# Kernel optimization log

Hardware: AMD Instinct MI355X
Metric: run time of the kernel (lower is better)

## Reference

```python
import jax, jax.numpy as jnp
import numpy as np
from jax import lax

DIM = 192
HEADS = 8
EPS = 1e-5


def setup_inputs() -> dict:
    key = jax.random.key(0)
    ks = jax.random.split(key, 8)
    B, C, H, W = 1, DIM, 64, 64
    x = jax.random.normal(ks[0], (B, C, H, W), dtype=jnp.float32)
    gamma = jnp.ones((C,), dtype=jnp.float32)
    beta = jnp.zeros((C,), dtype=jnp.float32)
    w_qkv = jax.random.normal(ks[1], (3 * C, C), dtype=jnp.float32) * (1.0 / np.sqrt(C))
    # depthwise 3x3 conv: (out_ch=3C, in_ch/groups=1, 3, 3), bias present (Conv2d default)
    w_dw = jax.random.normal(ks[2], (3 * C, 1, 3, 3), dtype=jnp.float32) * (1.0 / 3.0)
    b_dw = jax.random.normal(ks[3], (3 * C,), dtype=jnp.float32) * 0.01
    w_proj = jax.random.normal(ks[4], (C, C), dtype=jnp.float32) * (1.0 / np.sqrt(C))
    temperature = jnp.ones((HEADS, 1, 1), dtype=jnp.float32)
    return {"x": x, "gamma": gamma, "beta": beta, "w_qkv": w_qkv,
            "w_dw": w_dw, "b_dw": b_dw, "w_proj": w_proj,
            "temperature": temperature}


def _mdta(x, gamma, beta, w_qkv, w_dw, b_dw, w_proj, temperature):
    B, C, H, W = x.shape
    heads = HEADS
    d = C // heads
    N = H * W
    # LayerNorm over channel dim (applied on NHWC permute in torch)
    mean = jnp.mean(x, axis=1, keepdims=True)
    var = jnp.var(x, axis=1, keepdims=True)
    x_ln = (x - mean) * lax.rsqrt(var + EPS)
    x_ln = x_ln * gamma[None, :, None, None] + beta[None, :, None, None]
    # 1x1 conv (no bias): [B,3C,H,W]
    qkv = jnp.einsum('oc,bchw->bohw', w_qkv, x_ln)
    # depthwise 3x3 conv, padding=1, groups=3C
    qkv = lax.conv_general_dilated(
        qkv, w_dw, window_strides=(1, 1), padding=((1, 1), (1, 1)),
        dimension_numbers=('NCHW', 'OIHW', 'NCHW'),
        feature_group_count=3 * C)
    qkv = qkv + b_dw[None, :, None, None]
    q, k, v = jnp.split(qkv, 3, axis=1)
    q = q.reshape(B, heads, d, N)
    k = k.reshape(B, heads, d, N)
    v = v.reshape(B, heads, d, N)
    # attn[b,h,n,m] = sum_d q[b,h,d,n] k[b,h,d,m], scaled by learnable temperature
    attn = jnp.einsum('bhdn,bhdm->bhnm', q, k) * temperature  # (heads,1,1) broadcasts
    attn = jax.nn.softmax(attn, axis=-1)
    # out[b,h,d,n] = sum_m attn[b,h,n,m] v[b,h,d,m]
    out = jnp.einsum('bhnm,bhdm->bhdn', attn, v)
    out = out.reshape(B, C, H, W)
    out = jnp.einsum('oc,bchw->bohw', w_proj, out)
    return out + x


def reference(x, gamma, beta, w_qkv, w_dw, b_dw, w_proj, temperature):
    return _mdta(x, gamma, beta, w_qkv, w_dw, b_dw, w_proj, temperature)
```

## Files before the change

kernel.cpp:

```cpp
#include <hip/hip_runtime.h>
#include <hip/hip_bf16.h>


typedef __bf16 bf16;
typedef __bf16 bf16x2 __attribute__((ext_vector_type(2)));
typedef __bf16 bf16x4 __attribute__((ext_vector_type(4)));
typedef __bf16 bf16x8 __attribute__((ext_vector_type(8)));
typedef float f32x4 __attribute__((ext_vector_type(4)));

#define C_DIM 192
#define N_PIX 4096
#define HEADS 8
#define DHEAD 24
#define DPAD 32
#define C3 576
#define NSPLIT 8

__device__ inline float fast_exp2(float x) {
#if __has_builtin(__builtin_amdgcn_exp2f)
    return __builtin_amdgcn_exp2f(x);
#else
    return exp2f(x);
#endif
}

__device__ inline f32x4 mfma16(bf16x8 a, bf16x8 b, f32x4 c) {
    return __builtin_amdgcn_mfma_f32_16x16x32_bf16(a, b, c, 0, 0, 0);
}

__global__ __launch_bounds__(256) void ln_qkv(const float* __restrict__ x,
                                              const float* __restrict__ gamma,
                                              const float* __restrict__ beta,
                                              const float* __restrict__ wqkv,
                                              bf16* __restrict__ qkvb,
                                              float* __restrict__ maxk2) {
    __shared__ __align__(16) bf16 Bt[64 * 200];
    __shared__ float gs[C_DIM], bs[C_DIM];
    const int K = C_DIM;
    int n0 = blockIdx.x * 64;
    int m0 = blockIdx.y * 64;
    int t = threadIdx.x;
    if (t < C_DIM) { gs[t] = gamma[t]; bs[t] = beta[t]; }
    if (blockIdx.x == 0 && blockIdx.y == 0 && t < 8) maxk2[t] = 0.0f;
    __syncthreads();

    int lane = t & 63, wave = t >> 6;
    {
        int pl = wave * 16 + (lane & 15);
        int seg = lane >> 4;
        int p = n0 + pl;
        float v[48];
        float s = 0.f, ss = 0.f;
        for (int j = 0; j < 48; ++j) {
            float f = x[(seg * 48 + j) * N_PIX + p];
            v[j] = f; s += f; ss += f * f;
        }
        s += __shfl_xor(s, 16, 64); s += __shfl_xor(s, 32, 64);
        ss += __shfl_xor(ss, 16, 64); ss += __shfl_xor(ss, 32, 64);
        float mean = s * (1.0f / C_DIM);
        float var = ss * (1.0f / C_DIM) - mean * mean;
        float rstd = rsqrtf(var + 1e-5f);
        bf16* dst = Bt + pl * 200 + seg * 48;
        for (int g = 0; g < 6; ++g) {
            bf16x8 w;
            for (int j = 0; j < 8; ++j) {
                int c = seg * 48 + g * 8 + j;
                w[j] = (bf16)((v[g * 8 + j] - mean) * rstd * gs[c] + bs[c]);
            }
            *(bf16x8*)(dst + g * 8) = w;
        }
    }
    __syncthreads();

    int l16 = lane & 15, quad = lane >> 4;
    int wm = (wave >> 1) * 32, wn = (wave & 1) * 32;
    f32x4 acc[2][2] = {};
    for (int kk = 0; kk < K; kk += 32) {
        const f32x4* ar0 = (const f32x4*)(wqkv + (m0 + wm + l16) * K + kk + quad * 8);
        const f32x4* ar1 = (const f32x4*)(wqkv + (m0 + wm + 16 + l16) * K + kk + quad * 8);
        f32x4 w0a = ar0[0], w0b = ar0[1];
        f32x4 w1a = ar1[0], w1b = ar1[1];
        bf16x8 a0, a1;
        for (int j = 0; j < 4; ++j) {
            a0[j] = (bf16)w0a[j]; a0[4 + j] = (bf16)w0b[j];
            a1[j] = (bf16)w1a[j]; a1[4 + j] = (bf16)w1b[j];
        }
        bf16x8 b0 = *(const bf16x8*)(Bt + (wn + l16) * 200 + kk + quad * 8);
        bf16x8 b1 = *(const bf16x8*)(Bt + (wn + 16 + l16) * 200 + kk + quad * 8);
        acc[0][0] = mfma16(a0, b0, acc[0][0]);
        acc[0][1] = mfma16(a0, b1, acc[0][1]);
        acc[1][0] = mfma16(a1, b0, acc[1][0]);
        acc[1][1] = mfma16(a1, b1, acc[1][1]);
    }
    for (int i = 0; i < 2; ++i)
        for (int j = 0; j < 2; ++j)
            for (int r = 0; r < 4; ++r) {
                int row = m0 + wm + i * 16 + quad * 4 + r;
                int col = n0 + wn + j * 16 + l16;
                qkvb[(size_t)row * N_PIX + col] = (bf16)acc[i][j][r];
            }
}

__global__ __launch_bounds__(256) void dwconv(const bf16* __restrict__ qkv,
                                              const float* __restrict__ wdw,
                                              const float* __restrict__ bdw,
                                              bf16* __restrict__ qt,
                                              bf16* __restrict__ kt,
                                              bf16* __restrict__ vl,
                                              float* __restrict__ maxk2) {
    __shared__ float k2s[24][64];
    __shared__ bf16 stg[64 * DPAD];
    int bx = blockIdx.x;
    int part = bx >> 9;
    int h = (bx >> 6) & 7;
    int y = bx & 63;
    int t = threadIdx.x;
    int ch_local = t >> 3;
    int seg = t & 7;
    int px0 = seg * 8;
    bool active = ch_local < 24;

    float acc[8];
    if (active) {
        int ch = part * C_DIM + h * DHEAD + ch_local;
        const bf16* in = qkv + (size_t)ch * N_PIX;
        float w[9];
        for (int i = 0; i < 9; ++i) w[i] = wdw[ch * 9 + i];
        float bias = bdw[ch];
        float rowv[3][10];
        for (int r = 0; r < 3; ++r) {
            int yy = y + r - 1;
            if (yy >= 0 && yy < 64) {
                bf16x8 v8 = *(const bf16x8*)(in + yy * 64 + px0);
                for (int j = 0; j < 8; ++j) rowv[r][j + 1] = (float)v8[j];
                rowv[r][0] = (seg > 0) ? (float)in[yy * 64 + px0 - 1] : 0.f;
                rowv[r][9] = (seg < 7) ? (float)in[yy * 64 + px0 + 8] : 0.f;
            } else {
                for (int j = 0; j < 10; ++j) rowv[r][j] = 0.f;
            }
        }
        for (int j = 0; j < 8; ++j) {
            float a = bias;
            for (int r = 0; r < 3; ++r)
                a += w[r * 3 + 0] * rowv[r][j] + w[r * 3 + 1] * rowv[r][j + 1]
                   + w[r * 3 + 2] * rowv[r][j + 2];
            acc[j] = a;
        }
    }

    if (part == 2) {
        if (active) {
            bf16x8 v8;
            for (int j = 0; j < 8; ++j) v8[j] = (bf16)acc[j];
            *(bf16x8*)(vl + ((size_t)(h * DPAD + ch_local)) * N_PIX + y * 64 + px0) = v8;
        } else {
            int i = t - 192;
            int dd = 24 + (i >> 3);
            int s2 = i & 7;
            bf16 val = (bf16)((dd == 24) ? 1.0f : 0.0f);
            bf16x8 v8;
            for (int j = 0; j < 8; ++j) v8[j] = val;
            *(bf16x8*)(vl + ((size_t)(h * DPAD + dd)) * N_PIX + y * 64 + s2 * 8) = v8;
        }
    } else {
        if (active) {
            for (int j = 0; j < 8; ++j)
                stg[(px0 + j) * DPAD + ch_local] = (bf16)acc[j];
        } else {
            int i = t - 192;
            bf16x8 z;
            for (int j = 0; j < 8; ++j) z[j] = (bf16)0.0f;
            *(bf16x8*)(stg + i * DPAD + 24) = z;
        }
        if (part == 1 && active)
            for (int j = 0; j < 8; ++j) k2s[ch_local][px0 + j] = acc[j] * acc[j];
        __syncthreads();
        bf16* dst = (part == 0 ? qt : kt) + ((size_t)h * N_PIX + y * 64) * DPAD;
        *(bf16x8*)(dst + t * 8) = *(const bf16x8*)(stg + t * 8);
        if (part == 1 && t < 64) {
            float s = 0.f;
            for (int c = 0; c < 24; ++c) s += k2s[c][t];
            for (int off = 1; off < 64; off <<= 1)
                s = fmaxf(s, __shfl_xor(s, off, 64));
            if (t == 0) atomicMax((unsigned int*)(maxk2 + h), __float_as_uint(s));
        }
    }
}

__global__ __launch_bounds__(256, 4) void flash_attn(const bf16* __restrict__ qt,
                                                     const bf16* __restrict__ kt,
                                                     const bf16* __restrict__ vl,
                                                     const float* __restrict__ temp,
                                                     const float* __restrict__ maxk2,
                                                     bf16* __restrict__ opart,
                                                     bf16* __restrict__ lpart) {
    __shared__ __align__(16) bf16 Plds[16 * 1024];

    int tid = threadIdx.x;
    int wave = tid >> 6, lane = tid & 63;
    int l16 = lane & 15, quad = lane >> 4;
    int head = blockIdx.x & 7;
    int qb = (blockIdx.x >> 3) & 15;
    int split = blockIdx.x >> 7;
    int nbase = qb * 256 + wave * 64;
    float tl = temp[head] * 1.44269504f;

    const bf16* qrow = qt + ((size_t)head * N_PIX + nbase) * DPAD;
    bf16x8 aq[4];
    for (int f = 0; f < 4; ++f)
        aq[f] = *(const bf16x8*)(qrow + (size_t)(f * 16 + l16) * DPAD + quad * 8);

    float mk2 = maxk2[head];
    float Bb[4];
    for (int f = 0; f < 4; ++f) {
        float q2 = 0.f;
        for (int j = 0; j < 8; ++j) { float v = (float)aq[f][j]; q2 += v * v; }
        q2 += __shfl_xor(q2, 16, 64);
        q2 += __shfl_xor(q2, 32, 64);
        Bb[f] = fabsf(tl) * sqrtf(q2 * mk2) + 1.0f;
    }

    const bf16* kbase = kt + (size_t)head * N_PIX * DPAD;
    const bf16* vbase = vl + (size_t)head * DPAD * N_PIX;
    bf16* pw = Plds + wave * 4096;

    f32x4 o0[4] = {}, o1[4] = {};

    const int NITER = 64 / NSPLIT;
    int mbase = split * NITER * 64;

    bf16x8 ak[4];
    for (int mt = 0; mt < 4; ++mt)
        ak[mt] = *(const bf16x8*)(kbase + (size_t)(mbase + mt * 16 + l16) * DPAD + quad * 8);

    #pragma unroll 2
    for (int it = 0; it < NITER; ++it) {
        int m0 = mbase + it * 64;
        bf16x8 av0 = *(const bf16x8*)(vbase + (size_t)l16 * N_PIX + m0 + quad * 8);
        bf16x8 av1 = *(const bf16x8*)(vbase + (size_t)(16 + l16) * N_PIX + m0 + quad * 8);
        bf16x8 av2 = *(const bf16x8*)(vbase + (size_t)l16 * N_PIX + m0 + 32 + quad * 8);
        bf16x8 av3 = *(const bf16x8*)(vbase + (size_t)(16 + l16) * N_PIX + m0 + 32 + quad * 8);
        bf16x8 akn[4];
        if (it + 1 < NITER) {
            int m1 = m0 + 64;
            for (int mt = 0; mt < 4; ++mt)
                akn[mt] = *(const bf16x8*)(kbase + (size_t)(m1 + mt * 16 + l16) * DPAD + quad * 8);
        }

        for (int f = 0; f < 4; ++f) {
            bf16* pwf = pw + f * 1024;
            f32x4 z = {0.f, 0.f, 0.f, 0.f};
            f32x4 st[4];
            for (int mt = 0; mt < 4; ++mt) st[mt] = mfma16(ak[mt], aq[f], z);
            for (int mt = 0; mt < 4; ++mt) {
                bf16x4 pk;
                for (int r = 0; r < 4; ++r)
                    pk[r] = (bf16)fast_exp2(__builtin_fmaf(st[mt][r], tl, -Bb[f]));
                int chunk = mt * 2 + (quad >> 1);
                *(bf16x4*)(pwf + (chunk * 16 + l16) * 8 + (quad & 1) * 4) = pk;
            }
            bf16x8 ap0 = *(const bf16x8*)(pwf + (quad * 16 + l16) * 8);
            bf16x8 ap1 = *(const bf16x8*)(pwf + ((4 + quad) * 16 + l16) * 8);
            o0[f] = mfma16(av0, ap0, o0[f]);
            o1[f] = mfma16(av1, ap0, o1[f]);
            o0[f] = mfma16(av2, ap1, o0[f]);
            o1[f] = mfma16(av3, ap1, o1[f]);
        }
        if (it + 1 < NITER)
            for (int mt = 0; mt < 4; ++mt) ak[mt] = akn[mt];
    }

    for (int f = 0; f < 4; ++f) {
        int n = nbase + f * 16 + l16;
        size_t rowo = ((size_t)(split * 8 + head) * N_PIX + n) * 24;
        bf16x4 w0;
        for (int r = 0; r < 4; ++r) w0[r] = (bf16)o0[f][r];
        *(bf16x4*)(opart + rowo + quad * 4) = w0;
        if (quad < 2) {
            bf16x4 w1;
            for (int r = 0; r < 4; ++r) w1[r] = (bf16)o1[f][r];
            *(bf16x4*)(opart + rowo + 16 + quad * 4) = w1;
        }
        if (quad == 2)
            lpart[(size_t)(split * 8 + head) * N_PIX + n] = (bf16)o1[f][0];
    }
}

__global__ __launch_bounds__(256) void gemm_proj(const float* __restrict__ wproj,
                                                 const bf16* __restrict__ opart,
                                                 const bf16* __restrict__ lpart,
                                                 float* __restrict__ outf,
                                                 const float* __restrict__ resid) {
    __shared__ __align__(16) bf16 Bld[32 * 200];
    const int K = C_DIM;
    int n0 = blockIdx.x * 32;
    int m0 = blockIdx.y * 64;
    int t = threadIdx.x;
    {
        int h = t >> 5, nl = t & 31;
        int n = n0 + nl;
        float acc[24];
        for (int j = 0; j < 24; ++j) acc[j] = 0.f;
        float l = 0.f;
        for (int s = 0; s < NSPLIT; ++s) {
            const bf16* row = opart + ((size_t)(s * 8 + h) * N_PIX + n) * 24;
            bf16x8 a = *(const bf16x8*)(row);
            bf16x8 b = *(const bf16x8*)(row + 8);
            bf16x8 c = *(const bf16x8*)(row + 16);
            for (int j = 0; j < 8; ++j) {
                acc[j] += (float)a[j];
                acc[8 + j] += (float)b[j];
                acc[16 + j] += (float)c[j];
            }
            l += (float)lpart[(size_t)(s * 8 + h) * N_PIX + n];
        }
        float inv = 1.0f / l;
        bf16* dst = Bld + nl * 200 + h * 24;
        for (int g = 0; g < 3; ++g) {
            bf16x8 w;
            for (int j = 0; j < 8; ++j) w[j] = (bf16)(acc[g * 8 + j] * inv);
            *(bf16x8*)(dst + g * 8) = w;
        }
    }
    __syncthreads();
    int wave = t >> 6, lane = t & 63;
    int l16 = lane & 15, quad = lane >> 4;
    int mrow = m0 + wave * 16;
    float rv[8];
    for (int j = 0; j < 2; ++j)
        for (int r = 0; r < 4; ++r)
            rv[j * 4 + r] = resid[(size_t)(mrow + quad * 4 + r) * N_PIX + n0 + j * 16 + l16];
    f32x4 acc2[2] = {};
    for (int kk = 0; kk < K; kk += 32) {
        const f32x4* ar = (const f32x4*)(wproj + (mrow + l16) * K + kk + quad * 8);
        f32x4 wa = ar[0], wb = ar[1];
        bf16x8 a;
        for (int j = 0; j < 4; ++j) { a[j] = (bf16)wa[j]; a[4 + j] = (bf16)wb[j]; }
        bf16x8 b0 = *(const bf16x8*)(Bld + l16 * 200 + kk + quad * 8);
        bf16x8 b1 = *(const bf16x8*)(Bld + (16 + l16) * 200 + kk + quad * 8);
        acc2[0] = mfma16(a, b0, acc2[0]);
        acc2[1] = mfma16(a, b1, acc2[1]);
    }
    for (int j = 0; j < 2; ++j)
        for (int r = 0; r < 4; ++r) {
            int row = mrow + quad * 4 + r;
            int col = n0 + j * 16 + l16;
            outf[(size_t)row * N_PIX + col] = acc2[j][r] + rv[j * 4 + r];
        }
}

extern "C" void kernel_launch(void* const* d_in, const int* in_sizes, int n_in,
                              void* d_out, int out_size, void* d_ws, size_t ws_size,
                              hipStream_t stream) {
    const float* x     = (const float*)d_in[0];
    const float* gamma = (const float*)d_in[1];
    const float* beta  = (const float*)d_in[2];
    const float* wqkv  = (const float*)d_in[3];
    const float* wdw   = (const float*)d_in[4];
    const float* bdw   = (const float*)d_in[5];
    const float* wproj = (const float*)d_in[6];
    const float* temp  = (const float*)d_in[7];
    float* out = (float*)d_out;

    char* ws = (char*)d_ws;
    bf16* qkv     = (bf16*)(ws + 0);
    bf16* qt      = (bf16*)(ws + 4718592);
    bf16* kt      = (bf16*)(ws + 6815744);
    bf16* vl      = (bf16*)(ws + 8912896);
    bf16* opart   = (bf16*)(ws + 11010048);
    bf16* lpart   = (bf16*)(ws + 23592960);
    float* maxk2  = (float*)(ws + 24117248);

    ln_qkv<<<dim3(64, 9), 256, 0, stream>>>(x, gamma, beta, wqkv, qkv, maxk2);
    dwconv<<<1536, 256, 0, stream>>>(qkv, wdw, bdw, qt, kt, vl, maxk2);
    flash_attn<<<NSPLIT * 128, 256, 0, stream>>>(qt, kt, vl, temp, maxk2, opart, lpart);
    gemm_proj<<<dim3(128, 3), 256, 0, stream>>>(wproj, opart, lpart, out, x);
}
```

Baseline: 131.6 us.

## Keep softmax probabilities in registers by permuting V loads to match MFMA layout

Drops the per-wave LDS round trip that reshuffled exponentiated scores into the B-operand layout of the PV MFMA. The V fragments are now gathered with four 4-element loads per row so their key ordering matches the ordering the score accumulator already holds, letting P be packed directly from registers. This removes LDS writes, reads and the shared-memory allocation, which may also raise occupancy. In exchange the V loads become narrower, so there are more global load instructions per iteration.

```diff
diff --git a/kernel.cpp b/kernel.cpp
--- a/kernel.cpp
+++ b/kernel.cpp
@@ -194,8 +194,6 @@
                                                      const float* __restrict__ maxk2,
                                                      bf16* __restrict__ opart,
                                                      bf16* __restrict__ lpart) {
-    __shared__ __align__(16) bf16 Plds[16 * 1024];
-
     int tid = threadIdx.x;
     int wave = tid >> 6, lane = tid & 63;
     int l16 = lane & 15, quad = lane >> 4;
@@ -222,7 +220,6 @@
 
     const bf16* kbase = kt + (size_t)head * N_PIX * DPAD;
     const bf16* vbase = vl + (size_t)head * DPAD * N_PIX;
-    bf16* pw = Plds + wave * 4096;
 
     f32x4 o0[4] = {}, o1[4] = {};
 
@@ -236,10 +233,23 @@
     #pragma unroll 2
     for (int it = 0; it < NITER; ++it) {
         int m0 = mbase + it * 64;
-        bf16x8 av0 = *(const bf16x8*)(vbase + (size_t)l16 * N_PIX + m0 + quad * 8);
-        bf16x8 av1 = *(const bf16x8*)(vbase + (size_t)(16 + l16) * N_PIX + m0 + quad * 8);
-        bf16x8 av2 = *(const bf16x8*)(vbase + (size_t)l16 * N_PIX + m0 + 32 + quad * 8);
-        bf16x8 av3 = *(const bf16x8*)(vbase + (size_t)(16 + l16) * N_PIX + m0 + 32 + quad * 8);
+        const bf16* vr0 = vbase + (size_t)l16 * N_PIX + m0 + quad * 4;
+        const bf16* vr1 = vbase + (size_t)(16 + l16) * N_PIX + m0 + quad * 4;
+        bf16x4 v00 = *(const bf16x4*)(vr0);
+        bf16x4 v01 = *(const bf16x4*)(vr0 + 16);
+        bf16x4 v02 = *(const bf16x4*)(vr0 + 32);
+        bf16x4 v03 = *(const bf16x4*)(vr0 + 48);
+        bf16x4 v10 = *(const bf16x4*)(vr1);
+        bf16x4 v11 = *(const bf16x4*)(vr1 + 16);
+        bf16x4 v12 = *(const bf16x4*)(vr1 + 32);
+        bf16x4 v13 = *(const bf16x4*)(vr1 + 48);
+        bf16x8 av0, av1, av2, av3;
+        for (int j = 0; j < 4; ++j) {
+            av0[j] = v00[j]; av0[4 + j] = v01[j];
+            av1[j] = v10[j]; av1[4 + j] = v11[j];
+            av2[j] = v02[j]; av2[4 + j] = v03[j];
+            av3[j] = v12[j]; av3[4 + j] = v13[j];
+        }
         bf16x8 akn[4];
         if (it + 1 < NITER) {
             int m1 = m0 + 64;
@@ -248,19 +258,16 @@
         }
 
         for (int f = 0; f < 4; ++f) {
-            bf16* pwf = pw + f * 1024;
             f32x4 z = {0.f, 0.f, 0.f, 0.f};
             f32x4 st[4];
             for (int mt = 0; mt < 4; ++mt) st[mt] = mfma16(ak[mt], aq[f], z);
-            for (int mt = 0; mt < 4; ++mt) {
-                bf16x4 pk;
-                for (int r = 0; r < 4; ++r)
-                    pk[r] = (bf16)fast_exp2(__builtin_fmaf(st[mt][r], tl, -Bb[f]));
-                int chunk = mt * 2 + (quad >> 1);
-                *(bf16x4*)(pwf + (chunk * 16 + l16) * 8 + (quad & 1) * 4) = pk;
-            }
-            bf16x8 ap0 = *(const bf16x8*)(pwf + (quad * 16 + l16) * 8);
-            bf16x8 ap1 = *(const bf16x8*)(pwf + ((4 + quad) * 16 + l16) * 8);
+            bf16x8 ap0, ap1;
+            for (int r = 0; r < 4; ++r) {
+                ap0[r]     = (bf16)fast_exp2(__builtin_fmaf(st[0][r], tl, -Bb[f]));
+                ap0[4 + r] = (bf16)fast_exp2(__builtin_fmaf(st[1][r], tl, -Bb[f]));
+                ap1[r]     = (bf16)fast_exp2(__builtin_fmaf(st[2][r], tl, -Bb[f]));
+                ap1[4 + r] = (bf16)fast_exp2(__builtin_fmaf(st[3][r], tl, -Bb[f]));
+            }
             o0[f] = mfma16(av0, ap0, o0[f]);
             o1[f] = mfma16(av1, ap0, o1[f]);
             o0[f] = mfma16(av2, ap1, o0[f]);
```

Result: slower. 143.8 us (+9.3%).
